# Performance work log

Hardware: AMD Instinct MI355X
Metric: run time of the kernel (lower is better)

Reference implementation:

```python
import jax, jax.numpy as jnp
import numpy as np

SELF_TOPK_RATE = 0.05
LN_EPS = 1e-5


def _forward(q, k, v, fc_w, fc_b, ln_g, ln_b):
    # q, k, v: [B, S, D] (original code transposes to seq-first; math is identical batch-first)
    b, s, d = q.shape
    scale = d ** -0.5
    logits = jnp.einsum('bqd,bkd->bqk', q, k) * scale              # [B,S,S]
    # glbal_mask: self-similarity of keys, column-summed, top-k selection
    raw_self = jnp.einsum('bqd,bkd->bqk', k, k) * scale            # [B,S,S]
    w = raw_self.sum(axis=1)                                        # sum over dim=-2 -> [B,S]
    topk = max(1, int(s * SELF_TOPK_RATE))                          # static
    _, topk_idx = jax.lax.top_k(w, topk)                            # [B,topk]
    sel = jnp.zeros((b, s), dtype=bool).at[jnp.arange(b)[:, None], topk_idx].set(True)
    cmax = logits.max(axis=(1, 2))                                  # [B]
    w_mapped = jnp.where(sel, cmax[:, None], -cmax[:, None] / 3.0)  # [B,S]
    final = jax.nn.softmax(logits + w_mapped[:, None, :], axis=-1)  # [B,S,S]
    # Original einsum 'bqs,bkd->bqd' contracts s and k INDEPENDENTLY:
    # attn[b,q,d] = (sum_s final[b,q,s]) * (sum_k v[b,k,d])
    attn = final.sum(-1)[:, :, None] * v.sum(1)[:, None, :]         # [B,S,D]
    attn = jnp.nan_to_num(attn, nan=0.0, posinf=1e5, neginf=-1e5)
    h = attn @ fc_w.T + fc_b                                        # Linear; dropout = identity (eval)
    x = h + q                                                       # residual
    mu = x.mean(-1, keepdims=True)
    var = ((x - mu) ** 2).mean(-1, keepdims=True)
    return (x - mu) * jax.lax.rsqrt(var + LN_EPS) * ln_g + ln_b     # [B,S,D]


def setup_inputs() -> dict:
    key = jax.random.key(0)
    ks = jax.random.split(key, 5)
    B, S, D = 8, 2048, 768
    q = jax.random.normal(ks[0], (B, S, D), jnp.float32)
    k = jax.random.normal(ks[1], (B, S, D), jnp.float32)
    v = jax.random.normal(ks[2], (B, S, D), jnp.float32)
    mask = jnp.zeros((B, S), dtype=bool)  # unused in the original math path
    index = jnp.arange(B, dtype=jnp.int32)  # unused
    fc_w = jax.random.normal(ks[3], (D, D), jnp.float32) * 0.02
    fc_b = jnp.zeros((D,), jnp.float32)
    ln_g = jnp.ones((D,), jnp.float32)
    ln_b = jnp.zeros((D,), jnp.float32)
    return {"q": q, "k": k, "v": v, "mask": mask, "fc_w": fc_w, "fc_b": fc_b,
            "ln_g": ln_g, "ln_b": ln_b, "index": index, "typeAdd_Del": 1}


def reference(q, k, v, mask, fc_w, fc_b, ln_g, ln_b, index, typeAdd_Del):
    # mask, index, typeAdd_Del are accepted but unused by the original forward math
    return _forward(q, k, v, fc_w, fc_b, ln_g, ln_b)
```

## Files before the change

kernel.cpp:

```cpp
#include <hip/hip_runtime.h>
#include <hip/hip_cooperative_groups.h>

namespace cg = cooperative_groups;

#define NB 8
#define NS 2048
#define ND 768
#define ND4 192
#define SC 128
#define RPC 16
#define GRID 1024
#define TPB 256

typedef float f4 __attribute__((ext_vector_type(4)));

__device__ __forceinline__ void q_preload(const float* __restrict__ q,
                                          f4 qreg[12], int r0, int l) {
    const f4* qb = (const f4*)q + (size_t)r0 * ND4;
#pragma unroll
    for (int r = 0; r < 4; ++r)
#pragma unroll
        for (int k = 0; k < 3; ++k)
            qreg[r * 3 + k] = qb[(size_t)r * ND4 + l + k * 64];
}

__device__ __forceinline__ void ln_rows4(const f4 qreg[12],
                                         const float* __restrict__ hvec,
                                         const float* __restrict__ lng,
                                         const float* __restrict__ lnb,
                                         float* __restrict__ out,
                                         int b, int r0, int l) {
    const f4* h4 = (const f4*)hvec + (size_t)b * ND4;
    f4 h[3];
#pragma unroll
    for (int k = 0; k < 3; ++k) h[k] = h4[l + k * 64];

    float s[4], sq[4];
#pragma unroll
    for (int r = 0; r < 4; ++r) {
        s[r] = 0.f; sq[r] = 0.f;
#pragma unroll
        for (int k = 0; k < 3; ++k) {
            const f4 x = qreg[r * 3 + k] + h[k];
            s[r]  += x.x + x.y + x.z + x.w;
            sq[r] += x.x * x.x + x.y * x.y + x.z * x.z + x.w * x.w;
        }
    }
#pragma unroll
    for (int off = 32; off >= 1; off >>= 1)
#pragma unroll
        for (int r = 0; r < 4; ++r) {
            s[r]  += __shfl_xor(s[r],  off, 64);
            sq[r] += __shfl_xor(sq[r], off, 64);
        }
    const float inv = 1.0f / (float)ND;
    float mean[4], rstd[4];
#pragma unroll
    for (int r = 0; r < 4; ++r) {
        mean[r] = s[r] * inv;
        rstd[r] = rsqrtf(sq[r] * inv - mean[r] * mean[r] + 1e-5f);
    }
    f4* o4 = (f4*)out + (size_t)r0 * ND4;
#pragma unroll
    for (int k = 0; k < 3; ++k) {
        const int e4 = l + k * 64;
        const f4 gv = ((const f4*)lng)[e4];
        const f4 bv = ((const f4*)lnb)[e4];
#pragma unroll
        for (int r = 0; r < 4; ++r) {
            const f4 x = qreg[r * 3 + k] + h[k];
            f4 ov;
            ov.x = (x.x - mean[r]) * rstd[r] * gv.x + bv.x;
            ov.y = (x.y - mean[r]) * rstd[r] * gv.y + bv.y;
            ov.z = (x.z - mean[r]) * rstd[r] * gv.z + bv.z;
            ov.w = (x.w - mean[r]) * rstd[r] * gv.w + bv.w;
            __builtin_nontemporal_store(ov, o4 + (size_t)r * ND4 + e4);
        }
    }
}

__device__ __forceinline__ void bc_body(const float* __restrict__ part,
                                        const float* __restrict__ fcw,
                                        const float* __restrict__ fcb,
                                        float* __restrict__ hvec,
                                        float* __restrict__ lds_vs,
                                        int slab, int b, int t) {
    if (t < ND4) {
        const f4* p4 = (const f4*)part + (size_t)b * ND4 + t;
        f4 acc = (f4)(0.f);
#pragma unroll 8
        for (int c = 0; c < SC; ++c) acc += p4[(size_t)c * (NB * ND4)];
        ((f4*)lds_vs)[t] = acc;
    }
    __syncthreads();
    const int w = t >> 6, l = t & 63;
    const int g = l >> 4, li = l & 15;
#pragma unroll
    for (int it = 0; it < 6; ++it) {
        const int d = slab * 96 + w * 24 + it * 4 + g;
        const f4* wrow = (const f4*)(fcw + (size_t)d * ND);
        float s = 0.f;
#pragma unroll
        for (int j = 0; j < 12; ++j) {
            const int e4 = li + j * 16;
            const f4 wv = wrow[e4];
            const f4 vs = ((const f4*)lds_vs)[e4];
            s += wv.x * vs.x + wv.y * vs.y + wv.z * vs.z + wv.w * vs.w;
        }
        s += __shfl_xor(s, 1, 64); s += __shfl_xor(s, 2, 64);
        s += __shfl_xor(s, 4, 64); s += __shfl_xor(s, 8, 64);
        if (li == 0) hvec[b * ND + d] = s + fcb[d];
    }
}

__global__ __launch_bounds__(TPB, 4) void qreg_kernel(
    const float* __restrict__ q, const float* __restrict__ v,
    const float* __restrict__ fcw, const float* __restrict__ fcb,
    const float* __restrict__ lng, const float* __restrict__ lnb,
    float* __restrict__ part, float* __restrict__ hvec,
    float* __restrict__ out) {
    cg::grid_group grid = cg::this_grid();
    __shared__ float lds_vs[ND];
    const int bb = blockIdx.x, t = threadIdx.x;
    const int w = t >> 6, l = t & 63;
    const int r0 = bb * 16 + w * 4;
    const int bd = bb >> 7;

    f4 qreg[12];

    {
        const int c = bb >> 3, b = bb & 7;
        if (t < ND4) {
            const f4* v4 = (const f4*)v + ((size_t)(b * NS + c * RPC)) * ND4 + t;
            f4 acc = (f4)(0.f);
#pragma unroll
            for (int i = 0; i < RPC; ++i) acc += v4[(size_t)i * ND4];
            ((f4*)part)[((size_t)c * NB + b) * ND4 + t] = acc;
        }
        if (bb >= 64) q_preload(q, qreg, r0, l);
    }
    grid.sync();

    if (bb < 64) bc_body(part, fcw, fcb, hvec, lds_vs, bb >> 3, bb & 7, t);
    grid.sync();

    if (bb < 64) q_preload(q, qreg, r0, l);
    ln_rows4(qreg, hvec, lng, lnb, out, bd, r0, l);
}

__global__ __launch_bounds__(192) void vpart_kernel(const float* __restrict__ v,
                                                    float* __restrict__ part) {
    const int c = blockIdx.x, b = blockIdx.y, t = threadIdx.x;
    const f4* v4 = (const f4*)v + ((size_t)(b * NS + c * RPC)) * ND4 + t;
    f4 acc = (f4)(0.f);
#pragma unroll
    for (int i = 0; i < RPC; ++i) acc += v4[(size_t)i * ND4];
    ((f4*)part)[((size_t)c * NB + b) * ND4 + t] = acc;
}

__global__ __launch_bounds__(TPB) void bc_kernel(const float* __restrict__ part,
                                                 const float* __restrict__ fcw,
                                                 const float* __restrict__ fcb,
                                                 float* __restrict__ hvec) {
    __shared__ float lds_vs[ND];
    bc_body(part, fcw, fcb, hvec, lds_vs, blockIdx.x >> 3, blockIdx.x & 7, threadIdx.x);
}

__global__ __launch_bounds__(TPB) void ln_kernel(const float* __restrict__ q,
                                                 const float* __restrict__ hvec,
                                                 const float* __restrict__ lng,
                                                 const float* __restrict__ lnb,
                                                 float* __restrict__ out) {
    const int w = threadIdx.x >> 6, l = threadIdx.x & 63;
    const int r0 = blockIdx.x * 16 + w * 4;
    const int bd = r0 >> 11;
    f4 qreg[12];
    q_preload(q, qreg, r0, l);
    ln_rows4(qreg, hvec, lng, lnb, out, bd, r0, l);
}

extern "C" void kernel_launch(void* const* d_in, const int* in_sizes, int n_in,
                              void* d_out, int out_size, void* d_ws, size_t ws_size,
                              hipStream_t stream) {
    const float* q   = (const float*)d_in[0];
    const float* v   = (const float*)d_in[2];
    const float* fcw = (const float*)d_in[4];
    const float* fcb = (const float*)d_in[5];
    const float* lng = (const float*)d_in[6];
    const float* lnb = (const float*)d_in[7];
    float* out = (float*)d_out;

    float* part = (float*)d_ws;
    float* hvec = part + (size_t)SC * NB * ND;

    int blocksPerCU = 0;
    (void)hipOccupancyMaxActiveBlocksPerMultiprocessor(&blocksPerCU,
        (const void*)qreg_kernel, TPB, 0);
    static int numCU = 0;
    if (numCU == 0) {
        hipDeviceProp_t prop;
        (void)hipGetDeviceProperties(&prop, 0);
        numCU = prop.multiProcessorCount;
    }

    if (blocksPerCU * numCU >= GRID) {
        void* args[] = {(void*)&q, (void*)&v, (void*)&fcw, (void*)&fcb,
                        (void*)&lng, (void*)&lnb, (void*)&part, (void*)&hvec,
                        (void*)&out};
        (void)hipLaunchCooperativeKernel((const void*)qreg_kernel, dim3(GRID),
                                         dim3(TPB), args, 0, stream);
    } else {
        vpart_kernel<<<dim3(SC, NB), 192, 0, stream>>>(v, part);
        bc_kernel<<<64, TPB, 0, stream>>>(part, fcw, fcb, hvec);
        ln_kernel<<<GRID, TPB, 0, stream>>>(q, hvec, lng, lnb, out);
    }
}
```

Baseline: 47.13 us.

## Replace cooperative grid-sync kernel with atomic last-block fused reduction and LN kernel

Drops the cooperative kernel and its two grid-wide barriers. Work is now split into a v-column-sum kernel whose last eight blocks per batch, found through an atomic ticket counter, finish the reduction and run the FC matvec, followed by a separate LayerNorm kernel. The intent is to avoid the cost of grid synchronization and cooperative launch, and of running every block through the short FC phase. In exchange it adds a memset and a second kernel launch. It also loses the earlier overlap of q preloading with the v reduction, and the last blocks spin-wait on a global counter.

```diff
diff --git a/kernel.cpp b/kernel.cpp
--- a/kernel.cpp
+++ b/kernel.cpp
@@ -1,7 +1,4 @@
 #include <hip/hip_runtime.h>
-#include <hip/hip_cooperative_groups.h>
-
-namespace cg = cooperative_groups;
 
 #define NB 8
 #define NS 2048
@@ -9,27 +6,87 @@
 #define ND4 192
 #define SC 128
 #define RPC 16
-#define GRID 1024
-#define TPB 256
 
 typedef float f4 __attribute__((ext_vector_type(4)));
 
-__device__ __forceinline__ void q_preload(const float* __restrict__ q,
-                                          f4 qreg[12], int r0, int l) {
+__global__ __launch_bounds__(192) void vpart_bc_kernel(
+    const float* __restrict__ v, const float* __restrict__ fcw,
+    const float* __restrict__ fcb, float* __restrict__ part,
+    float* __restrict__ hvec, int* __restrict__ cnt) {
+    const int c = blockIdx.x, b = blockIdx.y, t = threadIdx.x;
+    __shared__ float lds_vs[ND];
+    __shared__ int ticket_s;
+
+    {
+        const f4* v4 = (const f4*)v + ((size_t)(b * NS + c * RPC)) * ND4 + t;
+        f4 acc = (f4)(0.f);
+#pragma unroll
+        for (int i = 0; i < RPC; ++i) acc += v4[(size_t)i * ND4];
+        ((f4*)part)[((size_t)c * NB + b) * ND4 + t] = acc;
+    }
+    __threadfence();
+    __syncthreads();
+    if (t == 0)
+        ticket_s = __hip_atomic_fetch_add(&cnt[b], 1, __ATOMIC_RELEASE,
+                                          __HIP_MEMORY_SCOPE_AGENT);
+    __syncthreads();
+    const int ticket = ticket_s;
+    if (ticket < SC - 8) return;
+    const int slab = ticket - (SC - 8);
+
+    if (t == 0)
+        while (__hip_atomic_load(&cnt[b], __ATOMIC_ACQUIRE,
+                                 __HIP_MEMORY_SCOPE_AGENT) < SC) {}
+    __syncthreads();
+
+    {
+        const f4* p4 = (const f4*)part + (size_t)b * ND4 + t;
+        f4 acc = (f4)(0.f);
+#pragma unroll 8
+        for (int cc = 0; cc < SC; ++cc) acc += p4[(size_t)cc * (NB * ND4)];
+        ((f4*)lds_vs)[t] = acc;
+    }
+    __syncthreads();
+
+    {
+        const int w = t >> 6, l = t & 63;
+        const int g = l >> 4, li = l & 15;
+#pragma unroll
+        for (int it = 0; it < 8; ++it) {
+            const int d = slab * 96 + w * 32 + it * 4 + g;
+            const f4* wrow = (const f4*)(fcw + (size_t)d * ND);
+            float s = 0.f;
+#pragma unroll
+            for (int j = 0; j < 12; ++j) {
+                const int e4 = li + j * 16;
+                const f4 wv = wrow[e4];
+                const f4 vs = ((const f4*)lds_vs)[e4];
+                s += wv.x * vs.x + wv.y * vs.y + wv.z * vs.z + wv.w * vs.w;
+            }
+            s += __shfl_xor(s, 1, 64); s += __shfl_xor(s, 2, 64);
+            s += __shfl_xor(s, 4, 64); s += __shfl_xor(s, 8, 64);
+            if (li == 0) hvec[b * ND + d] = s + fcb[d];
+        }
+    }
+}
+
+__global__ __launch_bounds__(256) void ln_kernel(const float* __restrict__ q,
+                                                 const float* __restrict__ hvec,
+                                                 const float* __restrict__ lng,
+                                                 const float* __restrict__ lnb,
+                                                 float* __restrict__ out) {
+    const int w = threadIdx.x >> 6, l = threadIdx.x & 63;
+    const int r0 = blockIdx.x * 16 + w * 4;
+    const int b = r0 >> 11;
+
     const f4* qb = (const f4*)q + (size_t)r0 * ND4;
+    f4 qreg[12];
 #pragma unroll
     for (int r = 0; r < 4; ++r)
 #pragma unroll
         for (int k = 0; k < 3; ++k)
             qreg[r * 3 + k] = qb[(size_t)r * ND4 + l + k * 64];
-}
 
-__device__ __forceinline__ void ln_rows4(const f4 qreg[12],
-                                         const float* __restrict__ hvec,
-                                         const float* __restrict__ lng,
-                                         const float* __restrict__ lnb,
-                                         float* __restrict__ out,
-                                         int b, int r0, int l) {
     const f4* h4 = (const f4*)hvec + (size_t)b * ND4;
     f4 h[3];
 #pragma unroll
@@ -79,106 +136,6 @@
     }
 }
 
-__device__ __forceinline__ void bc_body(const float* __restrict__ part,
-                                        const float* __restrict__ fcw,
-                                        const float* __restrict__ fcb,
-                                        float* __restrict__ hvec,
-                                        float* __restrict__ lds_vs,
-                                        int slab, int b, int t) {
-    if (t < ND4) {
-        const f4* p4 = (const f4*)part + (size_t)b * ND4 + t;
-        f4 acc = (f4)(0.f);
-#pragma unroll 8
-        for (int c = 0; c < SC; ++c) acc += p4[(size_t)c * (NB * ND4)];
-        ((f4*)lds_vs)[t] = acc;
-    }
-    __syncthreads();
-    const int w = t >> 6, l = t & 63;
-    const int g = l >> 4, li = l & 15;
-#pragma unroll
-    for (int it = 0; it < 6; ++it) {
-        const int d = slab * 96 + w * 24 + it * 4 + g;
-        const f4* wrow = (const f4*)(fcw + (size_t)d * ND);
-        float s = 0.f;
-#pragma unroll
-        for (int j = 0; j < 12; ++j) {
-            const int e4 = li + j * 16;
-            const f4 wv = wrow[e4];
-            const f4 vs = ((const f4*)lds_vs)[e4];
-            s += wv.x * vs.x + wv.y * vs.y + wv.z * vs.z + wv.w * vs.w;
-        }
-        s += __shfl_xor(s, 1, 64); s += __shfl_xor(s, 2, 64);
-        s += __shfl_xor(s, 4, 64); s += __shfl_xor(s, 8, 64);
-        if (li == 0) hvec[b * ND + d] = s + fcb[d];
-    }
-}
-
-__global__ __launch_bounds__(TPB, 4) void qreg_kernel(
-    const float* __restrict__ q, const float* __restrict__ v,
-    const float* __restrict__ fcw, const float* __restrict__ fcb,
-    const float* __restrict__ lng, const float* __restrict__ lnb,
-    float* __restrict__ part, float* __restrict__ hvec,
-    float* __restrict__ out) {
-    cg::grid_group grid = cg::this_grid();
-    __shared__ float lds_vs[ND];
-    const int bb = blockIdx.x, t = threadIdx.x;
-    const int w = t >> 6, l = t & 63;
-    const int r0 = bb * 16 + w * 4;
-    const int bd = bb >> 7;
-
-    f4 qreg[12];
-
-    {
-        const int c = bb >> 3, b = bb & 7;
-        if (t < ND4) {
-            const f4* v4 = (const f4*)v + ((size_t)(b * NS + c * RPC)) * ND4 + t;
-            f4 acc = (f4)(0.f);
-#pragma unroll
-            for (int i = 0; i < RPC; ++i) acc += v4[(size_t)i * ND4];
-            ((f4*)part)[((size_t)c * NB + b) * ND4 + t] = acc;
-        }
-        if (bb >= 64) q_preload(q, qreg, r0, l);
-    }
-    grid.sync();
-
-    if (bb < 64) bc_body(part, fcw, fcb, hvec, lds_vs, bb >> 3, bb & 7, t);
-    grid.sync();
-
-    if (bb < 64) q_preload(q, qreg, r0, l);
-    ln_rows4(qreg, hvec, lng, lnb, out, bd, r0, l);
-}
-
-__global__ __launch_bounds__(192) void vpart_kernel(const float* __restrict__ v,
-                                                    float* __restrict__ part) {
-    const int c = blockIdx.x, b = blockIdx.y, t = threadIdx.x;
-    const f4* v4 = (const f4*)v + ((size_t)(b * NS + c * RPC)) * ND4 + t;
-    f4 acc = (f4)(0.f);
-#pragma unroll
-    for (int i = 0; i < RPC; ++i) acc += v4[(size_t)i * ND4];
-    ((f4*)part)[((size_t)c * NB + b) * ND4 + t] = acc;
-}
-
-__global__ __launch_bounds__(TPB) void bc_kernel(const float* __restrict__ part,
-                                                 const float* __restrict__ fcw,
-                                                 const float* __restrict__ fcb,
-                                                 float* __restrict__ hvec) {
-    __shared__ float lds_vs[ND];
-    bc_body(part, fcw, fcb, hvec, lds_vs, blockIdx.x >> 3, blockIdx.x & 7, threadIdx.x);
-}
-
-__global__ __launch_bounds__(TPB) void ln_kernel(const float* __restrict__ q,
-                                                 const float* __restrict__ hvec,
-                                                 const float* __restrict__ lng,
-                                                 const float* __restrict__ lnb,
-                                                 float* __restrict__ out) {
-    const int w = threadIdx.x >> 6, l = threadIdx.x & 63;
-    const int r0 = blockIdx.x * 16 + w * 4;
-    const int bd = r0 >> 11;
-    f4 qreg[12];
-    q_preload(q, qreg, r0, l);
-    ln_rows4(qreg, hvec, lng, lnb, out, bd, r0, l);
-}
-
 extern "C" void kernel_launch(void* const* d_in, const int* in_sizes, int n_in,
                               void* d_out, int out_size, void* d_ws, size_t ws_size,
                               hipStream_t stream) {
@@ -192,26 +149,9 @@
 
     float* part = (float*)d_ws;
     float* hvec = part + (size_t)SC * NB * ND;
+    int*   cnt  = (int*)(hvec + NB * ND);
 
-    int blocksPerCU = 0;
-    (void)hipOccupancyMaxActiveBlocksPerMultiprocessor(&blocksPerCU,
-        (const void*)qreg_kernel, TPB, 0);
-    static int numCU = 0;
-    if (numCU == 0) {
-        hipDeviceProp_t prop;
-        (void)hipGetDeviceProperties(&prop, 0);
-        numCU = prop.multiProcessorCount;
-    }
-
-    if (blocksPerCU * numCU >= GRID) {
-        void* args[] = {(void*)&q, (void*)&v, (void*)&fcw, (void*)&fcb,
-                        (void*)&lng, (void*)&lnb, (void*)&part, (void*)&hvec,
-                        (void*)&out};
-        (void)hipLaunchCooperativeKernel((const void*)qreg_kernel, dim3(GRID),
-                                         dim3(TPB), args, 0, stream);
-    } else {
-        vpart_kernel<<<dim3(SC, NB), 192, 0, stream>>>(v, part);
-        bc_kernel<<<64, TPB, 0, stream>>>(part, fcw, fcb, hvec);
-        ln_kernel<<<GRID, TPB, 0, stream>>>(q, hvec, lng, lnb, out);
-    }
+    (void)hipMemsetAsync(cnt, 0, NB * sizeof(int), stream);
+    vpart_bc_kernel<<<dim3(SC, NB), 192, 0, stream>>>(v, fcw, fcb, part, hvec, cnt);
+    ln_kernel<<<(NB * NS) / 16, 256, 0, stream>>>(q, hvec, lng, lnb, out);
 }
```

Measured after the change: 150.8 us. +220.0%, slower.
